# Performance work log

Measured on AMD Instinct MI355X. Metric: run time of the kernel, lower is better.

Reference implementation:

```python
import jax, jax.numpy as jnp
import numpy as np

# --- model constants (cfg stand-ins) ---
V_TH = 1.0        # spike threshold
SURR_BETA = 0.2   # surrogate-gradient sigmoid slope
ALPHA_MEM = 0.9   # membrane leak
STP_DECAY = 0.95  # short-term plasticity recovery
STP_R = 0.3       # STP depression per spike
A_P = 0.01        # STDP potentiation amplitude (Abbott)
A_D = 0.012       # STDP depression amplitude (Abbott)

B, N, N_FF, D = 16, 2048, 512, 4  # batch, recurrent neurons, FF inputs, delays


def setup_inputs() -> dict:
    key = jax.random.key(0)
    ks = jax.random.split(key, 10)
    FF = jax.random.uniform(ks[0], (B, N_FF), dtype=jnp.float32)          # feedforward spikes/rates
    V = jax.random.normal(ks[1], (B, N), dtype=jnp.float32) * 0.5         # membrane potential
    th_adapt = jax.random.uniform(ks[2], (B, N), dtype=jnp.float32) * 0.2 # adaptive threshold (ALIF)
    Xbuf = (jax.random.uniform(ks[3], (D, B, N)) < 0.05).astype(jnp.float32)  # delayed spike buffer
    stp_state = jax.random.uniform(ks[4], (D, B, N), dtype=jnp.float32) * 0.1 - 0.05
    xbar_pre_int = jax.random.uniform(ks[5], (B, N), dtype=jnp.float32)   # presyn STDP trace (int)
    xbar_post = jax.random.uniform(ks[6], (B, N), dtype=jnp.float32)      # postsyn STDP trace
    xbar_pre_ff = jax.random.uniform(ks[7], (B, N_FF), dtype=jnp.float32) # presyn STDP trace (ff)
    W_int = jax.random.normal(ks[8], (N, N), dtype=jnp.float32) / np.sqrt(N)
    W_ff = jax.random.normal(ks[9], (N_FF, N), dtype=jnp.float32) / np.sqrt(N_FF)
    return dict(FF=FF, V=V, th_adapt=th_adapt, Xbuf=Xbuf, stp_state=stp_state,
                xbar_pre_int=xbar_pre_int, xbar_post=xbar_post, xbar_pre_ff=xbar_pre_ff,
                W_int=W_int, W_ff=W_ff)


def reference(FF, V, th_adapt, Xbuf, stp_state, xbar_pre_int, xbar_post, xbar_pre_ff, W_int, W_ff):
    # ALIFSpikes: spikes from membrane vs adaptive threshold (sigmoid surrogate),
    # delayed spikes Xd read from the circular buffer.
    X = jax.nn.sigmoid((V - (V_TH + th_adapt)) / SURR_BETA)          # [B,N]
    Xd = Xbuf                                                        # [D,B,N]

    # STP: per-presynaptic, per-delay short-term weight factor
    w_short = 1.0 + (stp_state * STP_DECAY - STP_R * Xd)             # [D,B,N]

    # Abbott STDP: pairwise pre/post trace modulation of base weights
    # w_long[b,i,j] = W[i,j] + A_P*xbar_pre[b,i]*X[b,j] - A_D*pre_spike[b,i]*xbar_post[b,j]
    w_long_int = (W_int[None]
                  + A_P * xbar_pre_int[:, :, None] * X[:, None, :]
                  - A_D * Xd[0][:, :, None] * xbar_post[:, None, :])  # [B,N,N]
    w_long_ff = (W_ff[None]
                 + A_P * xbar_pre_ff[:, :, None] * X[:, None, :]
                 - A_D * FF[:, :, None] * xbar_post[:, None, :])      # [B,N_FF,N]

    # DeltaSynapse: spike-gated, STP-modulated current accumulation
    current = (jnp.einsum('dbi,bij->bj', Xd * w_short, w_long_int)
               + jnp.einsum('bi,bij->bj', FF, w_long_ff))             # [B,N]

    # Membrane: leaky integration with reset-by-spike
    V_new = ALPHA_MEM * V * (1.0 - X) + current                      # [B,N]

    return jnp.stack([X, V_new])                                     # [2,B,N]
```

## Files before the change

### kernel.cpp

```cpp
#include <hip/hip_runtime.h>

#define BB 16
#define NN 2048
#define NFF 512
#define DD 4
#define BN (BB * NN)

#define ROWS 64
#define WR 16
#define YINT 32
#define YTOT 40
#define JC   256
#define NX   (NN / JC)

__global__ __launch_bounds__(256) void snn_gemv(
    const float* __restrict__ Wint, const float* __restrict__ Wff,
    const float* __restrict__ Xbuf, const float* __restrict__ stp,
    const float* __restrict__ FF,
    const float* __restrict__ xpre_int, const float* __restrict__ xpre_ff,
    float* __restrict__ part, float* __restrict__ scal_part)
{
    __shared__ __align__(16) float c_lds[BB * ROWS];
    __shared__ float4 red[2 * BB * 64];
    int x = blockIdx.x, y = blockIdx.y;
    int t = threadIdx.x;
    int w = t >> 6, l = t & 63;
    const float* Wm; int i0;

    if (y < YINT) {
        i0 = y * ROWS; Wm = Wint;
        #pragma unroll
        for (int bb = 0; bb < 4; ++bb) {
            int b = w * 4 + bb;
            int base = b * NN + i0 + l;
            float acc = 0.f;
            #pragma unroll
            for (int d = 0; d < DD; ++d) {
                float xd = Xbuf[d * BN + base];
                float s  = stp[d * BN + base];
                acc += xd * (1.f + 0.95f * s - 0.3f * xd);
            }
            c_lds[b * ROWS + l] = acc;
        }
    } else {
        i0 = (y - YINT) * ROWS; Wm = Wff;
        #pragma unroll
        for (int bb = 0; bb < 4; ++bb) {
            int b = w * 4 + bb;
            c_lds[b * ROWS + l] = FF[b * NFF + i0 + l];
        }
    }
    __syncthreads();

    if (x == 0) {
        #pragma unroll
        for (int bb = 0; bb < 4; ++bb) {
            int b = w * 4 + bb;
            float tv = c_lds[b * ROWS + l];
            float s0, s1;
            if (y < YINT) {
                s0 = tv * xpre_int[b * NN + i0 + l];
                s1 = tv * Xbuf[b * NN + i0 + l];
            } else {
                s0 = tv * xpre_ff[b * NFF + i0 + l];
                s1 = tv * tv;
            }
            #pragma unroll
            for (int o = 32; o; o >>= 1) { s0 += __shfl_xor(s0, o); s1 += __shfl_xor(s1, o); }
            if (l == 0) {
                scal_part[y * 32 + b]      = s0;
                scal_part[y * 32 + 16 + b] = s1;
            }
        }
    }

    int j0 = x * JC + l * 4;

    const float* wp = Wm + (size_t)(i0 + w * WR) * NN + j0;
    float4 buf[WR];
    #pragma unroll
    for (int r = 0; r < WR; ++r) buf[r] = *(const float4*)(wp + (size_t)r * NN);

    float4 acc[BB];
    #pragma unroll
    for (int b = 0; b < BB; ++b) acc[b] = make_float4(0.f, 0.f, 0.f, 0.f);

    #pragma unroll
    for (int rg = 0; rg < 4; ++rg) {
        float4 wv0 = buf[rg * 4 + 0], wv1 = buf[rg * 4 + 1];
        float4 wv2 = buf[rg * 4 + 2], wv3 = buf[rg * 4 + 3];
        int base = w * WR + rg * 4;
#define FMA16(b) { \
        float4 cr = *(const float4*)&c_lds[(b) * ROWS + base]; \
        acc[b].x += cr.x * wv0.x + cr.y * wv1.x + cr.z * wv2.x + cr.w * wv3.x; \
        acc[b].y += cr.x * wv0.y + cr.y * wv1.y + cr.z * wv2.y + cr.w * wv3.y; \
        acc[b].z += cr.x * wv0.z + cr.y * wv1.z + cr.z * wv2.z + cr.w * wv3.z; \
        acc[b].w += cr.x * wv0.w + cr.y * wv1.w + cr.z * wv2.w + cr.w * wv3.w; }
        FMA16(0)  FMA16(1)  FMA16(2)  FMA16(3)
        FMA16(4)  FMA16(5)  FMA16(6)  FMA16(7)
        FMA16(8)  FMA16(9)  FMA16(10) FMA16(11)
        FMA16(12) FMA16(13) FMA16(14) FMA16(15)
#undef FMA16
    }

    if (w >= 2) {
        float4* rb = &red[(w - 2) * BB * 64];
        #pragma unroll
        for (int b = 0; b < BB; ++b) rb[b * 64 + l] = acc[b];
    }
    __syncthreads();
    if (w < 2) {
        const float4* rb = &red[w * BB * 64];
        #pragma unroll
        for (int b = 0; b < BB; ++b) {
            float4 v = rb[b * 64 + l];
            acc[b].x += v.x; acc[b].y += v.y; acc[b].z += v.z; acc[b].w += v.w;
        }
    }
    __syncthreads();
    if (w == 1) {
        #pragma unroll
        for (int b = 0; b < BB; ++b) red[b * 64 + l] = acc[b];
    }
    __syncthreads();
    if (w == 0) {
        float* pp = part + (size_t)y * BN + j0;
        #pragma unroll
        for (int b = 0; b < BB; ++b) {
            float4 v = red[b * 64 + l];
            acc[b].x += v.x; acc[b].y += v.y; acc[b].z += v.z; acc[b].w += v.w;
            *(float4*)(pp + (size_t)b * NN) = acc[b];
        }
    }
}

__global__ __launch_bounds__(256) void snn_post(
    const float* __restrict__ V, const float* __restrict__ th,
    const float* __restrict__ xpost,
    const float* __restrict__ part, const float* __restrict__ scal_part,
    float* __restrict__ out_X, float* __restrict__ out_V)
{
    int idx = blockIdx.x * 256 + threadIdx.x;
    int b = idx >> 11;
    float c1 = 0.f, c2 = 0.f, c3 = 0.f, c4 = 0.f;
    #pragma unroll
    for (int y = 0; y < YINT; ++y) {
        c1 += scal_part[y * 32 + b];
        c2 += scal_part[y * 32 + 16 + b];
    }
    #pragma unroll
    for (int y = YINT; y < YTOT; ++y) {
        c3 += scal_part[y * 32 + b];
        c4 += scal_part[y * 32 + 16 + b];
    }
    float v = V[idx];
    float x = 1.f / (1.f + expf(-(v - 1.f - th[idx]) * 5.f));
    out_X[idx] = x;
    float s = 0.f;
    #pragma unroll
    for (int y = 0; y < YTOT; ++y) s += part[(size_t)y * BN + idx];
    float c = s + 0.01f * (c1 + c3) * x - 0.012f * (c2 + c4) * xpost[idx];
    out_V[idx] = 0.9f * v * (1.f - x) + c;
}

extern "C" void kernel_launch(void* const* d_in, const int* in_sizes, int n_in,
                              void* d_out, int out_size, void* d_ws, size_t ws_size,
                              hipStream_t stream) {
    const float* FF       = (const float*)d_in[0];
    const float* V        = (const float*)d_in[1];
    const float* th       = (const float*)d_in[2];
    const float* Xbuf     = (const float*)d_in[3];
    const float* stp      = (const float*)d_in[4];
    const float* xpre_int = (const float*)d_in[5];
    const float* xpost    = (const float*)d_in[6];
    const float* xpre_ff  = (const float*)d_in[7];
    const float* Wint     = (const float*)d_in[8];
    const float* Wff      = (const float*)d_in[9];
    float* out = (float*)d_out;
    float* ws  = (float*)d_ws;

    float* part = ws;
    float* sp   = ws + YTOT * BN;

    snn_gemv<<<dim3(NX, YTOT), 256, 0, stream>>>(
        Wint, Wff, Xbuf, stp, FF, xpre_int, xpre_ff, part, sp);

    snn_post<<<BN / 256, 256, 0, stream>>>(
        V, th, xpost, part, sp, out, out + BN);
}
```

Before: 18.77 us.

## Merge recurrent and feedforward weight rows into uniform 80-row slabs

The 2048 recurrent rows and 512 feedforward rows are now treated as one concatenated 2560-row matrix and split into 32 slabs of 80 rows, replacing the previous 40 slabs of 64 rows. Each wave holds 20 weight rows in registers instead of 16, and slabs that straddle the boundary mix both weight sources. Fewer slabs means fewer partial sums written to the workspace and read back in the post kernel, and a smaller grid (256 blocks versus 320). The cost is more registers per thread and per-row branching on the matrix source, which may lower occupancy.

```diff
diff --git a/kernel.cpp b/kernel.cpp
--- a/kernel.cpp
+++ b/kernel.cpp
@@ -6,10 +6,9 @@
 #define DD 4
 #define BN (BB * NN)
 
-#define ROWS 64
-#define WR 16
-#define YINT 32
-#define YTOT 40
+#define RS   80
+#define NSL  32
+#define WRR  20
 #define JC   256
 #define NX   (NN / JC)
 
@@ -20,78 +19,99 @@
     const float* __restrict__ xpre_int, const float* __restrict__ xpre_ff,
     float* __restrict__ part, float* __restrict__ scal_part)
 {
-    __shared__ __align__(16) float c_lds[BB * ROWS];
+    __shared__ __align__(16) float c_lds[BB * RS];
     __shared__ float4 red[2 * BB * 64];
-    int x = blockIdx.x, y = blockIdx.y;
+    int x = blockIdx.x, s = blockIdx.y;
     int t = threadIdx.x;
     int w = t >> 6, l = t & 63;
-    const float* Wm; int i0;
-
-    if (y < YINT) {
-        i0 = y * ROWS; Wm = Wint;
-        #pragma unroll
-        for (int bb = 0; bb < 4; ++bb) {
-            int b = w * 4 + bb;
-            int base = b * NN + i0 + l;
+    int g0 = s * RS;
+
+    #pragma unroll
+    for (int k = 0; k < 5; ++k) {
+        int e = k * 256 + t;
+        int b = e / RS, row = e - b * RS;
+        int grow = g0 + row;
+        float val;
+        if (grow < NN) {
+            int base = b * NN + grow;
             float acc = 0.f;
             #pragma unroll
             for (int d = 0; d < DD; ++d) {
                 float xd = Xbuf[d * BN + base];
-                float s  = stp[d * BN + base];
-                acc += xd * (1.f + 0.95f * s - 0.3f * xd);
-            }
-            c_lds[b * ROWS + l] = acc;
-        }
-    } else {
-        i0 = (y - YINT) * ROWS; Wm = Wff;
+                float sv = stp[d * BN + base];
+                acc += xd * (1.f + 0.95f * sv - 0.3f * xd);
+            }
+            val = acc;
+        } else {
+            val = FF[b * NFF + grow - NN];
+        }
+        c_lds[b * RS + row] = val;
+    }
+    __syncthreads();
+
+    if (x == 0) {
         #pragma unroll
         for (int bb = 0; bb < 4; ++bb) {
             int b = w * 4 + bb;
-            c_lds[b * ROWS + l] = FF[b * NFF + i0 + l];
-        }
-    }
-    __syncthreads();
-
-    if (x == 0) {
-        #pragma unroll
-        for (int bb = 0; bb < 4; ++bb) {
-            int b = w * 4 + bb;
-            float tv = c_lds[b * ROWS + l];
-            float s0, s1;
-            if (y < YINT) {
-                s0 = tv * xpre_int[b * NN + i0 + l];
-                s1 = tv * Xbuf[b * NN + i0 + l];
-            } else {
-                s0 = tv * xpre_ff[b * NFF + i0 + l];
-                s1 = tv * tv;
+            float s0i = 0.f, s1i = 0.f, s0f = 0.f, s1f = 0.f;
+            {
+                int row = l, grow = g0 + row;
+                float tv = c_lds[b * RS + row];
+                if (grow < NN) {
+                    s0i = tv * xpre_int[b * NN + grow];
+                    s1i = tv * Xbuf[b * NN + grow];
+                } else {
+                    s0f = tv * xpre_ff[b * NFF + grow - NN];
+                    s1f = tv * tv;
+                }
+            }
+            if (l < RS - 64) {
+                int row = 64 + l, grow = g0 + row;
+                float tv = c_lds[b * RS + row];
+                if (grow < NN) {
+                    s0i += tv * xpre_int[b * NN + grow];
+                    s1i += tv * Xbuf[b * NN + grow];
+                } else {
+                    s0f += tv * xpre_ff[b * NFF + grow - NN];
+                    s1f += tv * tv;
+                }
             }
             #pragma unroll
-            for (int o = 32; o; o >>= 1) { s0 += __shfl_xor(s0, o); s1 += __shfl_xor(s1, o); }
+            for (int o = 32; o; o >>= 1) {
+                s0i += __shfl_xor(s0i, o); s1i += __shfl_xor(s1i, o);
+                s0f += __shfl_xor(s0f, o); s1f += __shfl_xor(s1f, o);
+            }
             if (l == 0) {
-                scal_part[y * 32 + b]      = s0;
-                scal_part[y * 32 + 16 + b] = s1;
+                scal_part[s * 64 + 0 * BB + b] = s0i;
+                scal_part[s * 64 + 1 * BB + b] = s1i;
+                scal_part[s * 64 + 2 * BB + b] = s0f;
+                scal_part[s * 64 + 3 * BB + b] = s1f;
             }
         }
     }
 
     int j0 = x * JC + l * 4;
 
-    const float* wp = Wm + (size_t)(i0 + w * WR) * NN + j0;
-    float4 buf[WR];
-    #pragma unroll
-    for (int r = 0; r < WR; ++r) buf[r] = *(const float4*)(wp + (size_t)r * NN);
+    float4 buf[WRR];
+    #pragma unroll
+    for (int r = 0; r < WRR; ++r) {
+        int grow = g0 + w * WRR + r;
+        const float* src = (grow < NN) ? (Wint + (size_t)grow * NN)
+                                       : (Wff + (size_t)(grow - NN) * NN);
+        buf[r] = *(const float4*)(src + j0);
+    }
 
     float4 acc[BB];
     #pragma unroll
     for (int b = 0; b < BB; ++b) acc[b] = make_float4(0.f, 0.f, 0.f, 0.f);
 
     #pragma unroll
-    for (int rg = 0; rg < 4; ++rg) {
+    for (int rg = 0; rg < 5; ++rg) {
         float4 wv0 = buf[rg * 4 + 0], wv1 = buf[rg * 4 + 1];
         float4 wv2 = buf[rg * 4 + 2], wv3 = buf[rg * 4 + 3];
-        int base = w * WR + rg * 4;
+        int base = w * WRR + rg * 4;
 #define FMA16(b) { \
-        float4 cr = *(const float4*)&c_lds[(b) * ROWS + base]; \
+        float4 cr = *(const float4*)&c_lds[(b) * RS + base]; \
         acc[b].x += cr.x * wv0.x + cr.y * wv1.x + cr.z * wv2.x + cr.w * wv3.x; \
         acc[b].y += cr.x * wv0.y + cr.y * wv1.y + cr.z * wv2.y + cr.w * wv3.y; \
         acc[b].z += cr.x * wv0.z + cr.y * wv1.z + cr.z * wv2.z + cr.w * wv3.z; \
@@ -124,7 +144,7 @@
     }
     __syncthreads();
     if (w == 0) {
-        float* pp = part + (size_t)y * BN + j0;
+        float* pp = part + (size_t)s * BN + j0;
         #pragma unroll
         for (int b = 0; b < BB; ++b) {
             float4 v = red[b * 64 + l];
@@ -144,22 +164,19 @@
     int b = idx >> 11;
     float c1 = 0.f, c2 = 0.f, c3 = 0.f, c4 = 0.f;
     #pragma unroll
-    for (int y = 0; y < YINT; ++y) {
-        c1 += scal_part[y * 32 + b];
-        c2 += scal_part[y * 32 + 16 + b];
-    }
-    #pragma unroll
-    for (int y = YINT; y < YTOT; ++y) {
-        c3 += scal_part[y * 32 + b];
-        c4 += scal_part[y * 32 + 16 + b];
+    for (int s = 0; s < NSL; ++s) {
+        c1 += scal_part[s * 64 + 0 * BB + b];
+        c2 += scal_part[s * 64 + 1 * BB + b];
+        c3 += scal_part[s * 64 + 2 * BB + b];
+        c4 += scal_part[s * 64 + 3 * BB + b];
     }
     float v = V[idx];
     float x = 1.f / (1.f + expf(-(v - 1.f - th[idx]) * 5.f));
     out_X[idx] = x;
-    float s = 0.f;
-    #pragma unroll
-    for (int y = 0; y < YTOT; ++y) s += part[(size_t)y * BN + idx];
-    float c = s + 0.01f * (c1 + c3) * x - 0.012f * (c2 + c4) * xpost[idx];
+    float sum = 0.f;
+    #pragma unroll
+    for (int s = 0; s < NSL; ++s) sum += part[(size_t)s * BN + idx];
+    float c = sum + 0.01f * (c1 + c3) * x - 0.012f * (c2 + c4) * xpost[idx];
     out_V[idx] = 0.9f * v * (1.f - x) + c;
 }
 
@@ -180,9 +197,9 @@
     float* ws  = (float*)d_ws;
 
     float* part = ws;
-    float* sp   = ws + YTOT * BN;
-
-    snn_gemv<<<dim3(NX, YTOT), 256, 0, stream>>>(
+    float* sp   = ws + NSL * BN;
+
+    snn_gemv<<<dim3(NX, NSL), 256, 0, stream>>>(
         Wint, Wff, Xbuf, stp, FF, xpre_int, xpre_ff, part, sp);
 
     snn_post<<<BN / 256, 256, 0, stream>>>(
```

After: 21.03 us. 12.0% more time.
